# Kernel optimization log

Measured on AMD Instinct MI355X. Metric: run time of the kernel, lower is better.

Reference implementation:

```python
import jax, jax.numpy as jnp
import numpy as np

N_HEAD = 32
N_KV = 8
D = 2048
HD = D // N_HEAD
FF = 8192
EPS = 1e-5
THETA = 10000.0


def rms_norm(x, g):
    return g * x / jnp.sqrt(jnp.mean(x * x, axis=-1, keepdims=True) + EPS)


def rope(x):
    # x: [B, H, T, hd]; lucidrains interleaved RoPE
    T = x.shape[2]
    inv_freq = 1.0 / (THETA ** (jnp.arange(0, HD, 2, dtype=jnp.float32) / HD))  # [hd/2]
    freqs = jnp.arange(T, dtype=jnp.float32)[:, None] * inv_freq[None, :]       # [T, hd/2]
    freqs = jnp.repeat(freqs, 2, axis=-1)                                        # [T, hd]
    cos, sin = jnp.cos(freqs), jnp.sin(freqs)
    x1 = x[..., ::2]
    x2 = x[..., 1::2]
    rot = jnp.stack([-x2, x1], axis=-1).reshape(x.shape)
    return x * cos + rot * sin


def attention(x, wq, wk, wv, wo):
    B, T, C = x.shape
    q = (x @ wq).reshape(B, T, N_HEAD, HD).transpose(0, 2, 1, 3)  # [B,H,T,hd]
    k = (x @ wk).reshape(B, T, N_KV, HD).transpose(0, 2, 1, 3)    # [B,Hkv,T,hd]
    v = (x @ wv).reshape(B, T, N_KV, HD).transpose(0, 2, 1, 3)
    q = rope(q)
    k = rope(k)
    rep = N_HEAD // N_KV
    k = jnp.repeat(k, rep, axis=1)
    v = jnp.repeat(v, rep, axis=1)
    att = jnp.einsum('bhqd,bhkd->bhqk', q, k) * (1.0 / np.sqrt(HD))
    causal = jnp.tril(jnp.ones((T, T), dtype=bool))
    att = jnp.where(causal[None, None], att, -jnp.inf)
    att = jax.nn.softmax(att, axis=-1)
    y = jnp.einsum('bhqk,bhkd->bhqd', att, v)
    y = y.transpose(0, 2, 1, 3).reshape(B, T, C)
    return y @ wo


def mlp(x, wg, wu, wd):
    return (jax.nn.silu(x @ wg) * (x @ wu)) @ wd


def setup_inputs() -> dict:
    key = jax.random.key(0)
    ks = jax.random.split(key, 9)
    s = lambda fan_in: 1.0 / np.sqrt(fan_in)
    return {
        'x': jax.random.normal(ks[0], (1, 2048, D), dtype=jnp.float32),
        'g1': jnp.ones((D,), dtype=jnp.float32),
        'wq': jax.random.normal(ks[1], (D, D), dtype=jnp.float32) * s(D),
        'wk': jax.random.normal(ks[2], (D, N_KV * HD), dtype=jnp.float32) * s(D),
        'wv': jax.random.normal(ks[3], (D, N_KV * HD), dtype=jnp.float32) * s(D),
        'wo': jax.random.normal(ks[4], (D, D), dtype=jnp.float32) * s(D),
        'g2': jnp.ones((D,), dtype=jnp.float32),
        'wg': jax.random.normal(ks[5], (D, FF), dtype=jnp.float32) * s(D),
        'wu': jax.random.normal(ks[6], (D, FF), dtype=jnp.float32) * s(D),
        'wd': jax.random.normal(ks[7], (FF, D), dtype=jnp.float32) * s(FF),
    }


def reference(x, g1, wq, wk, wv, wo, g2, wg, wu, wd):
    residual = x
    x = rms_norm(x, g1)
    x = x + attention(x, wq, wk, wv, wo)
    x = rms_norm(x, g2)
    x = x + mlp(x, wg, wu, wd)
    x = x + residual
    return x
```

## Files before the change

kernel.cpp:

```cpp
#include <hip/hip_runtime.h>
#include <cstdint>
#include <cstddef>


typedef __attribute__((ext_vector_type(8))) short short8;
typedef __attribute__((ext_vector_type(4))) float f32x4;
typedef __attribute__((ext_vector_type(16))) float f32x16;

typedef __attribute__((address_space(1))) const void gvoid_t;
typedef __attribute__((address_space(3))) void lvoid_t;

__device__ inline unsigned short f2b(float f) {
  unsigned int u = __float_as_uint(f);
  u += 0x7fffu + ((u >> 16) & 1u);
  return (unsigned short)(u >> 16);
}
__device__ inline float b2f(unsigned short s) {
  return __uint_as_float((unsigned int)s << 16);
}
__device__ inline unsigned int pkbf(float lo, float hi) {
  unsigned int r;
  asm("v_cvt_pk_bf16_f32 %0, %1, %2" : "=v"(r) : "v"(lo), "v"(hi));
  return r;
}

__device__ inline void xcd_swz(int& bx, int& by) {
  const int nbx = gridDim.x;
  const int nwg = nbx * gridDim.y;
  int f = by * nbx + bx;
  f = (f & 7) * (nwg >> 3) + (f >> 3);
  bx = f % nbx;
  by = f / nbx;
}

__global__ __launch_bounds__(256) void transpose_cast(
    const float* __restrict__ W, unsigned short* __restrict__ Wt,
    int R, int ldW) {
  __shared__ unsigned short s[32 * 36];
  const int r0 = blockIdx.y * 32, c0 = blockIdx.x * 32;
  const int tr = threadIdx.x >> 3, tc = (threadIdx.x & 7) << 2;
  const float4 v = *(const float4*)(W + (size_t)(r0 + tr) * ldW + c0 + tc);
  s[tr * 36 + tc + 0] = f2b(v.x);
  s[tr * 36 + tc + 1] = f2b(v.y);
  s[tr * 36 + tc + 2] = f2b(v.z);
  s[tr * 36 + tc + 3] = f2b(v.w);
  __syncthreads();
  ushort4 o;
  o.x = s[(tc + 0) * 36 + tr];
  o.y = s[(tc + 1) * 36 + tr];
  o.z = s[(tc + 2) * 36 + tr];
  o.w = s[(tc + 3) * 36 + tr];
  *(ushort4*)(Wt + (size_t)(c0 + tr) * R + r0 + tc) = o;
}

__global__ __launch_bounds__(256) void rmsnorm(
    const float* __restrict__ X, const float* __restrict__ g,
    unsigned short* __restrict__ ob) {
  const int row = blockIdx.x;
  const float* x = X + (size_t)row * 2048;
  float ss = 0.f;
  for (int i = threadIdx.x; i < 2048; i += 256) { float v = x[i]; ss += v * v; }
  for (int off = 32; off; off >>= 1) ss += __shfl_down(ss, off, 64);
  __shared__ float red[4];
  if ((threadIdx.x & 63) == 0) red[threadIdx.x >> 6] = ss;
  __syncthreads();
  const float tot = red[0] + red[1] + red[2] + red[3];
  const float r = rsqrtf(tot * (1.f / 2048.f) + 1e-5f);
  for (int i = threadIdx.x; i < 2048; i += 256)
    ob[(size_t)row * 2048 + i] = f2b(x[i] * g[i] * r);
}

__global__ __launch_bounds__(256) void add_res(
    const unsigned short* __restrict__ h2, const float* __restrict__ x,
    float* __restrict__ out) {
  const int i = blockIdx.x * 256 + threadIdx.x;
  const ushort4 h = ((const ushort4*)h2)[i];
  const float4 xv = ((const float4*)x)[i];
  float4 o;
  o.x = xv.x + b2f(h.x); o.y = xv.y + b2f(h.y);
  o.z = xv.z + b2f(h.z); o.w = xv.w + b2f(h.w);
  ((float4*)out)[i] = o;
}

__global__ __launch_bounds__(256, 2) void gemm_bt(
    const unsigned short* __restrict__ A, const unsigned short* __restrict__ Bt,
    float* Cf, unsigned short* Cb,
    const unsigned short* add1b, const float* add2,
    int N, int Kfull, int Kchunk, int epi, int Tld,
    unsigned short* Cb2, unsigned short* Cb3) {
  __shared__ unsigned short As[128 * 64];
  __shared__ unsigned short Bs[128 * 64];
  const int tid = threadIdx.x;
  const int wave = tid >> 6, lane = tid & 63;
  const int quad = lane >> 4, l16 = lane & 15;
  int bx = blockIdx.x, by = blockIdx.y;
  xcd_swz(bx, by);
  const int m0 = by * 128, n0 = bx * 128;
  const int wr = (wave >> 1) * 64, wc = (wave & 1) * 64;
  const int Ks = blockIdx.z * Kchunk, Ke = Ks + Kchunk;

  f32x4 acc[4][4] = {};

  for (int k0 = Ks; k0 < Ke; k0 += 64) {
#pragma unroll
    for (int p = 0; p < 4; ++p) {
      const int idx = p * 256 + tid;
      const int row = idx >> 3;
      const int kc = ((idx & 7) ^ (row & 7)) * 8;
      const unsigned short* gA = A + (size_t)(m0 + row) * Kfull + k0 + kc;
      const unsigned short* gB = Bt + (size_t)(n0 + row) * Kfull + k0 + kc;
      unsigned short* lA = As + (size_t)(p * 256 + wave * 64) * 8;
      unsigned short* lB = Bs + (size_t)(p * 256 + wave * 64) * 8;
      __builtin_amdgcn_global_load_lds((gvoid_t*)gA, (lvoid_t*)lA, 16, 0, 0);
      __builtin_amdgcn_global_load_lds((gvoid_t*)gB, (lvoid_t*)lB, 16, 0, 0);
    }
    __syncthreads();

#pragma unroll
    for (int ks = 0; ks < 2; ++ks) {
      short8 af[4], bf[4];
#pragma unroll
      for (int i = 0; i < 4; ++i) {
        const int row = wr + i * 16 + l16;
        af[i] = *(const short8*)(As + row * 64 +
                                 (((ks << 2) | quad) ^ (row & 7)) * 8);
      }
#pragma unroll
      for (int j = 0; j < 4; ++j) {
        const int row = wc + j * 16 + l16;
        bf[j] = *(const short8*)(Bs + row * 64 +
                                 (((ks << 2) | quad) ^ (row & 7)) * 8);
      }
#pragma unroll
      for (int i = 0; i < 4; ++i)
#pragma unroll
        for (int j = 0; j < 4; ++j)
          acc[i][j] = __builtin_amdgcn_mfma_f32_16x16x32_bf16(
              af[i], bf[j], acc[i][j], 0, 0, 0);
    }
    __syncthreads();
  }

  if (epi == 7 && n0 >= 2560) {
#pragma unroll
    for (int i = 0; i < 4; ++i)
#pragma unroll
      for (int j = 0; j < 4; ++j) {
        const int row = m0 + wr + i * 16 + quad * 4;
        const int col = n0 + wc + j * 16 + l16 - 2560;
        ushort4 o;
        o.x = f2b(acc[i][j][0]); o.y = f2b(acc[i][j][1]);
        o.z = f2b(acc[i][j][2]); o.w = f2b(acc[i][j][3]);
        *(ushort4*)(Cb3 + (size_t)col * Tld + row) = o;
      }
    return;
  }

#pragma unroll
  for (int i = 0; i < 4; ++i)
#pragma unroll
    for (int j = 0; j < 4; ++j) {
      const int rowb = m0 + wr + i * 16 + quad * 4;
      const int col = n0 + wc + j * 16 + l16;
      float invf = 0.f, sgn = 0.f;
      if (epi == 7) {
        const int ip = (col & 63) >> 1;
        invf = __expf(-(float)ip * 0.28782313662f);
        sgn = (col & 1) ? 1.f : -1.f;
      }
#pragma unroll
      for (int r = 0; r < 4; ++r) {
        const size_t idx = (size_t)(rowb + r) * N + col;
        const float v = acc[i][j][r];
        const float p = __shfl_xor(v, 1, 64);
        if (epi == 1) {
          Cf[idx] = v + b2f(add1b[idx]);
        } else if (epi == 8) {
          atomicAdd(&Cf[idx], v);
        } else if (epi == 4) {
          Cb[idx] = f2b(v);
        } else if (epi == 3) {
          const float gt = b2f(add1b[idx]);
          Cb[idx] = f2b(gt / (1.f + __expf(-gt)) * v);
        } else {
          float sn, cs;
          __sincosf((float)(rowb + r) * invf, &sn, &cs);
          const unsigned short o = f2b(v * cs + sgn * p * sn);
          if (col < 2048)
            Cb[(size_t)(rowb + r) * 2048 + col] = o;
          else
            Cb2[(size_t)(rowb + r) * 512 + col - 2048] = o;
        }
      }
    }
}

__global__ __launch_bounds__(256, 2) void gemm_gu(
    const unsigned short* __restrict__ A, const unsigned short* __restrict__ Bg,
    const unsigned short* __restrict__ Bu, unsigned short* __restrict__ act,
    int N, int K) {
  __shared__ unsigned short As[128 * 64];
  __shared__ unsigned short Gs[128 * 64];
  __shared__ unsigned short Us[128 * 64];
  const int tid = threadIdx.x;
  const int wave = tid >> 6, lane = tid & 63;
  const int quad = lane >> 4, l16 = lane & 15;
  int bx = blockIdx.x, by = blockIdx.y;
  xcd_swz(bx, by);
  const int m0 = by * 128, n0 = bx * 128;
  const int wr = (wave >> 1) * 64, wc = (wave & 1) * 64;

  f32x4 aG[4][4] = {}, aU[4][4] = {};

  for (int k0 = 0; k0 < K; k0 += 64) {
#pragma unroll
    for (int p = 0; p < 4; ++p) {
      const int idx = p * 256 + tid;
      const int row = idx >> 3;
      const int kc = ((idx & 7) ^ (row & 7)) * 8;
      const size_t off = (size_t)(p * 256 + wave * 64) * 8;
      __builtin_amdgcn_global_load_lds(
          (gvoid_t*)(A + (size_t)(m0 + row) * K + k0 + kc),
          (lvoid_t*)(As + off), 16, 0, 0);
      __builtin_amdgcn_global_load_lds(
          (gvoid_t*)(Bg + (size_t)(n0 + row) * K + k0 + kc),
          (lvoid_t*)(Gs + off), 16, 0, 0);
      __builtin_amdgcn_global_load_lds(
          (gvoid_t*)(Bu + (size_t)(n0 + row) * K + k0 + kc),
          (lvoid_t*)(Us + off), 16, 0, 0);
    }
    __syncthreads();

#pragma unroll
    for (int ks = 0; ks < 2; ++ks) {
      short8 af[4], bg[4], bu[4];
#pragma unroll
      for (int i = 0; i < 4; ++i) {
        const int row = wr + i * 16 + l16;
        af[i] = *(const short8*)(As + row * 64 +
                                 (((ks << 2) | quad) ^ (row & 7)) * 8);
      }
#pragma unroll
      for (int j = 0; j < 4; ++j) {
        const int row = wc + j * 16 + l16;
        const int kk = (((ks << 2) | quad) ^ (row & 7)) * 8;
        bg[j] = *(const short8*)(Gs + row * 64 + kk);
        bu[j] = *(const short8*)(Us + row * 64 + kk);
      }
#pragma unroll
      for (int i = 0; i < 4; ++i)
#pragma unroll
        for (int j = 0; j < 4; ++j) {
          aG[i][j] = __builtin_amdgcn_mfma_f32_16x16x32_bf16(
              af[i], bg[j], aG[i][j], 0, 0, 0);
          aU[i][j] = __builtin_amdgcn_mfma_f32_16x16x32_bf16(
              af[i], bu[j], aU[i][j], 0, 0, 0);
        }
    }
    __syncthreads();
  }

#pragma unroll
  for (int i = 0; i < 4; ++i)
#pragma unroll
    for (int j = 0; j < 4; ++j) {
      const int rowb = m0 + wr + i * 16 + quad * 4;
      const int col = n0 + wc + j * 16 + l16;
#pragma unroll
      for (int r = 0; r < 4; ++r) {
        const float g = aG[i][j][r], u = aU[i][j][r];
        act[(size_t)(rowb + r) * N + col] = f2b(g / (1.f + __expf(-g)) * u);
      }
    }
}

__global__ __launch_bounds__(256) void flash_attn(
    const unsigned short* __restrict__ Qb, const unsigned short* __restrict__ Kb,
    const unsigned short* __restrict__ Vt, unsigned short* __restrict__ Y,
    int T) {
  const int tid = threadIdx.x;
  const int wave = tid >> 6, lane = tid & 63;
  const int l32 = lane & 31, hi = lane >> 5;
  const int h = blockIdx.y, kvh = h >> 2;
  const int qt = (blockIdx.x + wave * 16) << 5;
  const int qrow = qt + l32;

  short8 qf[4];
#pragma unroll
  for (int ds = 0; ds < 4; ++ds) {
    short8 v = *(const short8*)(Qb + (size_t)qrow * 2048 + h * 64 +
                                ds * 16 + hi * 8);
#pragma unroll
    for (int e = 0; e < 8; ++e)
      v[e] = (short)f2b(b2f((unsigned short)v[e]) * 0.125f);
    qf[ds] = v;
  }

  const unsigned short* Kp = Kb + (size_t)l32 * 512 + kvh * 64 + hi * 8;
  const unsigned short* Vp = Vt + (size_t)(kvh * 64 + l32) * T + hi * 8;

  const int niter = (qt >> 5) + 1;
  float m_i = -3e38f, l_i = 0.f;
  f32x16 o0 = {}, o1 = {};

  short8 kf[4], kfn[4];
#pragma unroll
  for (int ds = 0; ds < 4; ++ds) kf[ds] = *(const short8*)(Kp + ds * 16);

  for (int it = 0; it < niter; ++it) {
    const int k0 = it << 5;
    short8 vf[2][2];
#pragma unroll
    for (int dt = 0; dt < 2; ++dt)
#pragma unroll
      for (int ks = 0; ks < 2; ++ks)
        vf[dt][ks] =
            *(const short8*)(Vp + (size_t)dt * 32 * T + k0 + ks * 16);
    const int kn = (k0 + 32 < 2016) ? k0 + 32 : 2016;
#pragma unroll
    for (int ds = 0; ds < 4; ++ds)
      kfn[ds] = *(const short8*)(Kp + (size_t)kn * 512 + ds * 16);

    f32x16 S = {};
#pragma unroll
    for (int ds = 0; ds < 4; ++ds)
      S = __builtin_amdgcn_mfma_f32_32x32x16_bf16(kf[ds], qf[ds], S, 0, 0, 0);

    float s[16];
#pragma unroll
    for (int r = 0; r < 16; ++r) s[r] = S[r];
    if (k0 == qt) {
#pragma unroll
      for (int r = 0; r < 16; ++r)
        if (((r & 3) + 8 * (r >> 2) + 4 * hi) > l32) s[r] = -3e38f;
    }

    float tmax = s[0];
#pragma unroll
    for (int r = 1; r < 16; ++r) tmax = fmaxf(tmax, s[r]);
    tmax = fmaxf(tmax, __shfl_xor(tmax, 32, 64));

    if (!__all(tmax <= m_i + 8.f)) {
      const float mn = fmaxf(m_i, tmax);
      const float al = __expf(m_i - mn);
#pragma unroll
      for (int r = 0; r < 16; ++r) { o0[r] *= al; o1[r] *= al; }
      l_i *= al;
      m_i = mn;
    }

    float p[16], rs = 0.f;
#pragma unroll
    for (int r = 0; r < 16; ++r) { p[r] = __expf(s[r] - m_i); rs += p[r]; }
    rs += __shfl_xor(rs, 32, 64);
    l_i += rs;

    short8 pf[2];
#pragma unroll
    for (int ks = 0; ks < 2; ++ks) {
      const int rb = ks * 8;
      const unsigned int a0 = pkbf(p[rb + 0], p[rb + 1]);
      const unsigned int a1 = pkbf(p[rb + 2], p[rb + 3]);
      const unsigned int b0 = pkbf(p[rb + 4], p[rb + 5]);
      const unsigned int b1 = pkbf(p[rb + 6], p[rb + 7]);
      const unsigned int t0 = __shfl_xor((int)(hi ? a0 : b0), 32, 64);
      const unsigned int t1 = __shfl_xor((int)(hi ? a1 : b1), 32, 64);
      union { unsigned int u[4]; short8 v; } pu;
      pu.u[0] = hi ? t0 : a0;
      pu.u[1] = hi ? t1 : a1;
      pu.u[2] = hi ? b0 : t0;
      pu.u[3] = hi ? b1 : t1;
      pf[ks] = pu.v;
    }

#pragma unroll
    for (int ks = 0; ks < 2; ++ks) {
      o0 = __builtin_amdgcn_mfma_f32_32x32x16_bf16(vf[0][ks], pf[ks], o0,
                                                   0, 0, 0);
      o1 = __builtin_amdgcn_mfma_f32_32x32x16_bf16(vf[1][ks], pf[ks], o1,
                                                   0, 0, 0);
    }
#pragma unroll
    for (int ds = 0; ds < 4; ++ds) kf[ds] = kfn[ds];
  }

  const float inv = 1.f / l_i;
  unsigned short* Yp = Y + (size_t)qrow * 2048 + h * 64 + hi * 4;
#pragma unroll
  for (int g = 0; g < 4; ++g) {
    ushort4 u0, u1;
    u0.x = f2b(o0[g * 4 + 0] * inv); u0.y = f2b(o0[g * 4 + 1] * inv);
    u0.z = f2b(o0[g * 4 + 2] * inv); u0.w = f2b(o0[g * 4 + 3] * inv);
    *(ushort4*)(Yp + g * 8) = u0;
    u1.x = f2b(o1[g * 4 + 0] * inv); u1.y = f2b(o1[g * 4 + 1] * inv);
    u1.z = f2b(o1[g * 4 + 2] * inv); u1.w = f2b(o1[g * 4 + 3] * inv);
    *(ushort4*)(Yp + 32 + g * 8) = u1;
  }
}

extern "C" void kernel_launch(void* const* d_in, const int* in_sizes, int n_in,
                              void* d_out, int out_size, void* d_ws,
                              size_t ws_size, hipStream_t stream) {
  const float* x  = (const float*)d_in[0];
  const float* g1 = (const float*)d_in[1];
  const float* wq = (const float*)d_in[2];
  const float* wk = (const float*)d_in[3];
  const float* wv = (const float*)d_in[4];
  const float* wo = (const float*)d_in[5];
  const float* g2 = (const float*)d_in[6];
  const float* wg = (const float*)d_in[7];
  const float* wu = (const float*)d_in[8];
  const float* wd = (const float*)d_in[9];
  float* out = (float*)d_out;

  const int T = 2048, Dm = 2048, FF = 8192;
  char* ws = (char*)d_ws;
  const size_t MB = (size_t)1 << 20;

  unsigned short* wq_t = (unsigned short*)(ws + 0 * MB);
  unsigned short* wk_t = (unsigned short*)(ws + 8 * MB);
  unsigned short* wv_t = (unsigned short*)(ws + 10 * MB);
  unsigned short* wo_t = (unsigned short*)(ws + 12 * MB);
  unsigned short* wg_t = (unsigned short*)(ws + 20 * MB);
  unsigned short* wu_t = (unsigned short*)(ws + 52 * MB);
  unsigned short* h1_b = (unsigned short*)(ws + 84 * MB);
  unsigned short* h2_b = (unsigned short*)(ws + 92 * MB);
  float*          x2_f = (float*)(ws + 100 * MB);
  unsigned short* gate = (unsigned short*)(ws + 100 * MB);
  unsigned short* q_b  = (unsigned short*)(ws + 132 * MB);
  unsigned short* k_b  = (unsigned short*)(ws + 140 * MB);
  unsigned short* vt_b = (unsigned short*)(ws + 142 * MB);
  unsigned short* y_b  = (unsigned short*)(ws + 144 * MB);
  unsigned short* wd_t = (unsigned short*)(ws + 132 * MB);

  transpose_cast<<<dim3(64, 64), 256, 0, stream>>>(wq, wq_t, Dm, Dm);
  transpose_cast<<<dim3(16, 64), 256, 0, stream>>>(wk, wk_t, Dm, 512);
  transpose_cast<<<dim3(16, 64), 256, 0, stream>>>(wv, wv_t, Dm, 512);
  transpose_cast<<<dim3(64, 64), 256, 0, stream>>>(wo, wo_t, Dm, Dm);
  transpose_cast<<<dim3(256, 64), 256, 0, stream>>>(wg, wg_t, Dm, FF);
  transpose_cast<<<dim3(256, 64), 256, 0, stream>>>(wu, wu_t, Dm, FF);

  rmsnorm<<<T, 256, 0, stream>>>(x, g1, h1_b);

  gemm_bt<<<dim3(24, 16), 256, 0, stream>>>(h1_b, wq_t, nullptr, q_b, nullptr,
                                            nullptr, 3072, Dm, Dm, 7, T, k_b,
                                            vt_b);

  flash_attn<<<dim3(16, 32), 256, 0, stream>>>(q_b, k_b, vt_b, y_b, T);

  gemm_bt<<<dim3(16, 16), 256, 0, stream>>>(y_b, wo_t, x2_f, nullptr, h1_b,
                                            nullptr, Dm, Dm, Dm, 1, 0, nullptr,
                                            nullptr);

  transpose_cast<<<dim3(64, 256), 256, 0, stream>>>(wd, wd_t, FF, Dm);

  rmsnorm<<<T, 256, 0, stream>>>(x2_f, g2, h2_b);

  gemm_gu<<<dim3(64, 16), 256, 0, stream>>>(h2_b, wg_t, wu_t, gate, FF, Dm);

  add_res<<<(T * Dm / 4) / 256, 256, 0, stream>>>(h2_b, x, out);
  gemm_bt<<<dim3(16, 16, 4), 256, 0, stream>>>(gate, wd_t, out, nullptr,
                                               nullptr, nullptr, Dm, FF,
                                               FF / 4, 8, 0, nullptr, nullptr);
}
```

Measured before the change: 724.7 us.

## Partition tiles by XCD column blocks and split-K the output projection

Replaces the XCD swizzle with a mapping that gives each XCD a contiguous band of N-columns, which should improve L2 reuse of B tiles within an XCD. The output projection GEMM becomes 2-way split-K with atomic accumulation into a buffer pre-filled with the bf16 residual, so more workgroups are in flight. The down-projection split-K drops from 4 to 2, halving atomic traffic. Unused epilogue branches are removed. The cost is an extra prefill kernel and atomic adds on the attention output path.

Measured after the change: 702.3 us. 3.1% less time.

```diff
diff --git a/kernel.cpp b/kernel.cpp
--- a/kernel.cpp
+++ b/kernel.cpp
@@ -24,13 +24,14 @@
   return r;
 }
 
-__device__ inline void xcd_swz(int& bx, int& by) {
-  const int nbx = gridDim.x;
-  const int nwg = nbx * gridDim.y;
-  int f = by * nbx + bx;
-  f = (f & 7) * (nwg >> 3) + (f >> 3);
-  bx = f % nbx;
-  by = f / nbx;
+__device__ inline void xcd_part(int& bx, int& by) {
+  const int nbx = gridDim.x, nby = gridDim.y;
+  const int cpx = nbx >> 3;
+  const int f = by * nbx + bx;
+  const int xcd = f & 7;
+  const int t = f >> 3;
+  bx = xcd * cpx + t / nby;
+  by = t % nby;
 }
 
 __global__ __launch_bounds__(256) void transpose_cast(
@@ -82,6 +83,15 @@
   ((float4*)out)[i] = o;
 }
 
+__global__ __launch_bounds__(256) void prefill_b2f(
+    const unsigned short* __restrict__ h, float* __restrict__ out) {
+  const int i = blockIdx.x * 256 + threadIdx.x;
+  const ushort4 v = ((const ushort4*)h)[i];
+  float4 o;
+  o.x = b2f(v.x); o.y = b2f(v.y); o.z = b2f(v.z); o.w = b2f(v.w);
+  ((float4*)out)[i] = o;
+}
+
 __global__ __launch_bounds__(256, 2) void gemm_bt(
     const unsigned short* __restrict__ A, const unsigned short* __restrict__ Bt,
     float* Cf, unsigned short* Cb,
@@ -94,7 +104,7 @@
   const int wave = tid >> 6, lane = tid & 63;
   const int quad = lane >> 4, l16 = lane & 15;
   int bx = blockIdx.x, by = blockIdx.y;
-  xcd_swz(bx, by);
+  xcd_part(bx, by);
   const int m0 = by * 128, n0 = bx * 128;
   const int wr = (wave >> 1) * 64, wc = (wave & 1) * 64;
   const int Ks = blockIdx.z * Kchunk, Ke = Ks + Kchunk;
@@ -177,11 +187,6 @@
           Cf[idx] = v + b2f(add1b[idx]);
         } else if (epi == 8) {
           atomicAdd(&Cf[idx], v);
-        } else if (epi == 4) {
-          Cb[idx] = f2b(v);
-        } else if (epi == 3) {
-          const float gt = b2f(add1b[idx]);
-          Cb[idx] = f2b(gt / (1.f + __expf(-gt)) * v);
         } else {
           float sn, cs;
           __sincosf((float)(rowb + r) * invf, &sn, &cs);
@@ -206,7 +211,7 @@
   const int wave = tid >> 6, lane = tid & 63;
   const int quad = lane >> 4, l16 = lane & 15;
   int bx = blockIdx.x, by = blockIdx.y;
-  xcd_swz(bx, by);
+  xcd_part(bx, by);
   const int m0 = by * 128, n0 = bx * 128;
   const int wr = (wave >> 1) * 64, wc = (wave & 1) * 64;
 
@@ -448,9 +453,10 @@
 
   flash_attn<<<dim3(16, 32), 256, 0, stream>>>(q_b, k_b, vt_b, y_b, T);
 
-  gemm_bt<<<dim3(16, 16), 256, 0, stream>>>(y_b, wo_t, x2_f, nullptr, h1_b,
-                                            nullptr, Dm, Dm, Dm, 1, 0, nullptr,
-                                            nullptr);
+  prefill_b2f<<<(T * Dm / 4) / 256, 256, 0, stream>>>(h1_b, x2_f);
+  gemm_bt<<<dim3(16, 16, 2), 256, 0, stream>>>(y_b, wo_t, x2_f, nullptr,
+                                               nullptr, nullptr, Dm, Dm,
+                                               Dm / 2, 8, 0, nullptr, nullptr);
 
   transpose_cast<<<dim3(64, 256), 256, 0, stream>>>(wd, wd_t, FF, Dm);
 
@@ -459,7 +465,7 @@
   gemm_gu<<<dim3(64, 16), 256, 0, stream>>>(h2_b, wg_t, wu_t, gate, FF, Dm);
 
   add_res<<<(T * Dm / 4) / 256, 256, 0, stream>>>(h2_b, x, out);
-  gemm_bt<<<dim3(16, 16, 4), 256, 0, stream>>>(gate, wd_t, out, nullptr,
+  gemm_bt<<<dim3(16, 16, 2), 256, 0, stream>>>(gate, wd_t, out, nullptr,
                                                nullptr, nullptr, Dm, FF,
-                                               FF / 4, 8, 0, nullptr, nullptr);
-}
+                                               FF / 2, 8, 0, nullptr, nullptr);
+}
```
